# Kernel optimization log

Measured on AMD Instinct MI355X. Metric: run time of the kernel, lower is better.

The kernel has to match this reference:

```python
import jax, jax.numpy as jnp
import numpy as np

B, S, D = 32, 512, 768
V = 8192          # codebook size
K = 8             # mixing samples per position
DP_NOISE_SCALE = 0.1


def setup_inputs() -> dict:
    key = jax.random.key(0)
    k1, k2, k3, k4 = jax.random.split(key, 4)
    base_embeddings = jax.random.normal(k1, (B, S, D), dtype=jnp.float32)
    codebook = jax.random.normal(k2, (V, D), dtype=jnp.float32)
    # stands in for the torch Laplace(0, dp_noise_scale) sample; unit-scale laplace here,
    # scaled by DP_NOISE_SCALE inside reference
    noise = jax.random.laplace(k3, (B, S, D), dtype=jnp.float32)
    # stands in for np.random.randint(batch_size) drawn per (b, s, k)
    rand_idx = jax.random.randint(k4, (B, S, K), 0, B, dtype=jnp.int32)
    return {"base_embeddings": base_embeddings, "codebook": codebook,
            "noise": noise, "rand_idx": rand_idx}


def reference(base_embeddings, codebook, noise, rand_idx):
    # --- VQ quantize: nearest codebook entry per token -----------------
    cb_sq = jnp.sum(codebook * codebook, axis=-1)              # [V]
    dots = jnp.einsum('bsd,vd->bsv', base_embeddings, codebook)  # [B,S,V]
    idx = jnp.argmin(cb_sq[None, None, :] - 2.0 * dots, axis=-1)  # [B,S] int

    # --- random cross-batch mixing of codebook vectors -----------------
    # mixed[b,s] = mean_j codebook[ idx[rand_idx[b,s,j], s] ]
    s_ar = jnp.arange(S)[None, :, None]                         # [1,S,1]
    gathered_idx = idx[rand_idx, s_ar]                          # [B,S,K]
    mixed = jnp.mean(codebook[gathered_idx], axis=2)            # [B,S,D]

    # --- DP laplace noise ----------------------------------------------
    mixed = mixed + DP_NOISE_SCALE * noise
    return mixed
```

## Files before the change

### kernel.cpp

```cpp
#include <hip/hip_runtime.h>
#include <hip/hip_bf16.h>
#include <cstdint>

#define BB 32
#define SS 512
#define DD 768
#define VV 8192
#define KK 8
#define TT (BB * SS)
#define NOISE_SCALE 0.1f

#define BM 128
#define BN 128
#define BK 32
#define NS 8
#define NTL ((VV / NS) / BN)
#define NKC (DD / BK)
#define DELTA 0.25f

using short8  = __attribute__((ext_vector_type(8))) short;
using ushort8 = __attribute__((ext_vector_type(8))) unsigned short;
using f32x4   = __attribute__((ext_vector_type(4))) float;

__global__ void cbsq_kernel(const float* __restrict__ cb, float* __restrict__ cbsq) {
    int row  = blockIdx.x * 4 + (threadIdx.x >> 6);
    int lane = threadIdx.x & 63;
    const float4* p = reinterpret_cast<const float4*>(cb + (size_t)row * DD);
    float s = 0.f;
#pragma unroll
    for (int w = 0; w < 3; ++w) {
        float4 v = p[lane + 64 * w];
        s += v.x * v.x + v.y * v.y + v.z * v.z + v.w * v.w;
    }
#pragma unroll
    for (int off = 32; off; off >>= 1) s += __shfl_xor(s, off, 64);
    if (lane == 0) cbsq[row] = s;
}

__device__ __forceinline__ void top2_ins(float s, int n, float& s1, int& i1,
                                         float& s2, int& i2) {
    if (s < s1 || (s == s1 && n < i1)) { s2 = s1; i2 = i1; s1 = s; i1 = n; }
    else if (s < s2 || (s == s2 && n < i2)) { s2 = s; i2 = n; }
}

__device__ __forceinline__ void bfsplit(float v, unsigned short& h, unsigned short& l) {
    uint u = __float_as_uint(v);
    h = (unsigned short)(u >> 16);
    float r = v - __uint_as_float(u & 0xffff0000u);
    l = (unsigned short)(__float_as_uint(r) >> 16);
}

__device__ __forceinline__ int swz(int row, int slot) {
    return slot ^ ((row ^ (row >> 2)) & 3);
}

__global__ __launch_bounds__(256) void conv_kernel(
    const float* __restrict__ src, unsigned short* __restrict__ hi,
    unsigned short* __restrict__ lo) {
    int i = blockIdx.x * 256 + threadIdx.x;
    float4 v = reinterpret_cast<const float4*>(src)[i];
    ushort4 h, l;
    bfsplit(v.x, h.x, l.x); bfsplit(v.y, h.y, l.y);
    bfsplit(v.z, h.z, l.z); bfsplit(v.w, h.w, l.w);
    reinterpret_cast<ushort4*>(hi)[i] = h;
    reinterpret_cast<ushort4*>(lo)[i] = l;
}

template <bool PRECONV>
__global__ __launch_bounds__(256, 2) void argmin_mfma(
    const float* __restrict__ X,
    const float* __restrict__ CB,
    const unsigned short* __restrict__ Xh, const unsigned short* __restrict__ Xl,
    const unsigned short* __restrict__ CBh, const unsigned short* __restrict__ CBl,
    const float* __restrict__ cbsq,
    float4* __restrict__ part)
{
    __shared__ unsigned short Ah[BM * BK], Al[BM * BK], Bh[BM * BK], Bl[BM * BK];

    const int tid  = threadIdx.x;
    const int lane = tid & 63;
    const int wid  = tid >> 6;
    const int wm = wid >> 1, wn = wid & 1;
    const int l15 = lane & 15, lg = lane >> 4;
    const int mtile = blockIdx.x >> 3;
    const int ns    = blockIdx.x & 7;
    const int m0 = mtile * BM;

    float s1[16], s2[16]; int i1[16], i2[16];
#pragma unroll
    for (int j = 0; j < 16; ++j) {
        s1[j] = INFINITY; s2[j] = INFINITY; i1[j] = 0x7fffffff; i2[j] = 0x7fffffff;
    }

    for (int nt = 0; nt < NTL; ++nt) {
        const int n1 = ns * (VV / NS) + nt * BN;

        f32x4 acc[4][4];
#pragma unroll
        for (int mt = 0; mt < 4; ++mt)
#pragma unroll
            for (int nf = 0; nf < 4; ++nf) acc[mt][nf] = (f32x4){0.f, 0.f, 0.f, 0.f};

        for (int kc = 0; kc < NKC; ++kc) {
            if constexpr (PRECONV) {
                const unsigned short* Agh = Xh  + (size_t)m0 * DD + kc * BK;
                const unsigned short* Agl = Xl  + (size_t)m0 * DD + kc * BK;
                const unsigned short* Bgh = CBh + (size_t)n1 * DD + kc * BK;
                const unsigned short* Bgl = CBl + (size_t)n1 * DD + kc * BK;
#pragma unroll
                for (int i = 0; i < 2; ++i) {
                    int e = tid + 256 * i;
                    int row = e >> 2, q = e & 3;
                    int so = row * BK + (swz(row, q) << 3);
                    size_t go = (size_t)row * DD + q * 8;
                    *reinterpret_cast<ushort8*>(&Ah[so]) = *reinterpret_cast<const ushort8*>(Agh + go);
                    *reinterpret_cast<ushort8*>(&Al[so]) = *reinterpret_cast<const ushort8*>(Agl + go);
                    *reinterpret_cast<ushort8*>(&Bh[so]) = *reinterpret_cast<const ushort8*>(Bgh + go);
                    *reinterpret_cast<ushort8*>(&Bl[so]) = *reinterpret_cast<const ushort8*>(Bgl + go);
                }
            } else {
                const float* Ag = X  + (size_t)m0 * DD + kc * BK;
                const float* Bg = CB + (size_t)n1 * DD + kc * BK;
#pragma unroll
                for (int i = 0; i < 4; ++i) {
                    int e = tid + 256 * i;
                    int row = e >> 3, kq = (e & 7) << 2;
                    int so = row * BK + (swz(row, kq >> 3) << 3) + (kq & 7);
                    float4 va = *reinterpret_cast<const float4*>(Ag + (size_t)row * DD + kq);
                    ushort4 ha, la;
                    bfsplit(va.x, ha.x, la.x); bfsplit(va.y, ha.y, la.y);
                    bfsplit(va.z, ha.z, la.z); bfsplit(va.w, ha.w, la.w);
                    *reinterpret_cast<ushort4*>(&Ah[so]) = ha;
                    *reinterpret_cast<ushort4*>(&Al[so]) = la;
                    float4 vb = *reinterpret_cast<const float4*>(Bg + (size_t)row * DD + kq);
                    ushort4 hb, lb;
                    bfsplit(vb.x, hb.x, lb.x); bfsplit(vb.y, hb.y, lb.y);
                    bfsplit(vb.z, hb.z, lb.z); bfsplit(vb.w, hb.w, lb.w);
                    *reinterpret_cast<ushort4*>(&Bh[so]) = hb;
                    *reinterpret_cast<ushort4*>(&Bl[so]) = lb;
                }
            }
            __syncthreads();

            short8 ah[4], al[4];
#pragma unroll
            for (int mt = 0; mt < 4; ++mt) {
                int row = wm * 64 + mt * 16 + l15;
                int fo  = row * BK + (swz(row, lg) << 3);
                ah[mt] = *reinterpret_cast<const short8*>(&Ah[fo]);
                al[mt] = *reinterpret_cast<const short8*>(&Al[fo]);
            }
#pragma unroll
            for (int nf = 0; nf < 4; ++nf) {
                int row = wn * 64 + nf * 16 + l15;
                int fo  = row * BK + (swz(row, lg) << 3);
                short8 bh = *reinterpret_cast<const short8*>(&Bh[fo]);
                short8 bl = *reinterpret_cast<const short8*>(&Bl[fo]);
#pragma unroll
                for (int mt = 0; mt < 4; ++mt) {
                    acc[mt][nf] = __builtin_amdgcn_mfma_f32_16x16x32_bf16(ah[mt], bh, acc[mt][nf], 0, 0, 0);
                    acc[mt][nf] = __builtin_amdgcn_mfma_f32_16x16x32_bf16(ah[mt], bl, acc[mt][nf], 0, 0, 0);
                    acc[mt][nf] = __builtin_amdgcn_mfma_f32_16x16x32_bf16(al[mt], bh, acc[mt][nf], 0, 0, 0);
                }
            }
            __syncthreads();
        }

        float cq[4]; int nn[4];
#pragma unroll
        for (int nf = 0; nf < 4; ++nf) {
            nn[nf] = n1 + wn * 64 + nf * 16 + l15;
            cq[nf] = cbsq[nn[nf]];
        }
#pragma unroll
        for (int mt = 0; mt < 4; ++mt)
#pragma unroll
            for (int r = 0; r < 4; ++r) {
                const int j = mt * 4 + r;
#pragma unroll
                for (int nf = 0; nf < 4; ++nf) {
                    float s = fmaf(-2.f, acc[mt][nf][r], cq[nf]);
                    top2_ins(s, nn[nf], s1[j], i1[j], s2[j], i2[j]);
                }
            }
    }

#pragma unroll
    for (int st = 1; st < 16; st <<= 1) {
#pragma unroll
        for (int j = 0; j < 16; ++j) {
            float os1 = __shfl_xor(s1[j], st, 64); int oi1 = __shfl_xor(i1[j], st, 64);
            float os2 = __shfl_xor(s2[j], st, 64); int oi2 = __shfl_xor(i2[j], st, 64);
            top2_ins(os1, oi1, s1[j], i1[j], s2[j], i2[j]);
            top2_ins(os2, oi2, s1[j], i1[j], s2[j], i2[j]);
        }
    }
    if (l15 == 0) {
#pragma unroll
        for (int j = 0; j < 16; ++j) {
            int mt = j >> 2, r = j & 3;
            int token = m0 + wm * 64 + mt * 16 + lg * 4 + r;
            part[(size_t)(ns * 2 + wn) * TT + token] =
                make_float4(s1[j], s2[j], __int_as_float(i1[j]), __int_as_float(i2[j]));
        }
    }
}

__global__ __launch_bounds__(256) void rescue_kernel(
    const float* __restrict__ X, const float* __restrict__ CB,
    const float* __restrict__ cbsq, const float4* __restrict__ part,
    int* __restrict__ idx)
{
    int wv = threadIdx.x >> 6, lane = threadIdx.x & 63;
    int t = blockIdx.x * 4 + wv;

    float s1 = INFINITY, s2 = INFINITY; int j1 = 0x7fffffff, j2 = 0x7fffffff;
    if (lane < 16) {
        float4 p = part[(size_t)lane * TT + t];
        s1 = p.x; s2 = p.y; j1 = __float_as_int(p.z); j2 = __float_as_int(p.w);
    }
#pragma unroll
    for (int st = 1; st < 16; st <<= 1) {
        float os1 = __shfl_xor(s1, st, 64); int oi1 = __shfl_xor(j1, st, 64);
        float os2 = __shfl_xor(s2, st, 64); int oi2 = __shfl_xor(j2, st, 64);
        top2_ins(os1, oi1, s1, j1, s2, j2);
        top2_ins(os2, oi2, s1, j1, s2, j2);
    }
    s1 = __shfl(s1, 0, 64); s2 = __shfl(s2, 0, 64);
    j1 = __shfl(j1, 0, 64); j2 = __shfl(j2, 0, 64);

    int res;
    if (s2 - s1 > DELTA) {
        res = j1;
    } else {
        const float* x  = X  + (size_t)t * DD;
        const float* c1 = CB + (size_t)j1 * DD;
        const float* c2 = CB + (size_t)j2 * DD;
        float p1 = 0.f, p2 = 0.f;
#pragma unroll
        for (int q = 0; q < 12; ++q) {
            int d = lane + 64 * q;
            p1 = fmaf(x[d], c1[d], p1);
            p2 = fmaf(x[d], c2[d], p2);
        }
#pragma unroll
        for (int off = 32; off; off >>= 1) {
            p1 += __shfl_xor(p1, off, 64);
            p2 += __shfl_xor(p2, off, 64);
        }
        float e1 = fmaf(-2.f, p1, cbsq[j1]);
        float e2 = fmaf(-2.f, p2, cbsq[j2]);
        res = (e1 < e2 || (e1 == e2 && j1 < j2)) ? j1 : j2;
    }
    if (lane == 0) idx[t] = res;
}

__global__ __launch_bounds__(256) void mix_kernel(
    const float* __restrict__ CB,
    const float* __restrict__ noise,
    const int*   __restrict__ ridx,
    const int*   __restrict__ idx,
    float* __restrict__ out)
{
    int wave = threadIdx.x >> 6;
    int lane = threadIdx.x & 63;
    int t = blockIdx.x * 4 + wave;
    int s = t & (SS - 1);

    const int* r = ridx + (size_t)t * KK;
    const float4* nz = reinterpret_cast<const float4*>(noise + (size_t)t * DD);
    float4* o = reinterpret_cast<float4*>(out + (size_t)t * DD);

    const float4* rows[KK];
#pragma unroll
    for (int j = 0; j < KK; ++j) {
        int g = idx[r[j] * SS + s];
        rows[j] = reinterpret_cast<const float4*>(CB + (size_t)g * DD);
    }

#pragma unroll
    for (int w = 0; w < 3; ++w) {
        int p = lane + 64 * w;
        float4 a = {0.f, 0.f, 0.f, 0.f};
#pragma unroll
        for (int j = 0; j < KK; ++j) {
            float4 c = rows[j][p];
            a.x += c.x; a.y += c.y; a.z += c.z; a.w += c.w;
        }
        float4 nv = nz[p];
        float4 res;
        res.x = a.x * 0.125f + NOISE_SCALE * nv.x;
        res.y = a.y * 0.125f + NOISE_SCALE * nv.y;
        res.z = a.z * 0.125f + NOISE_SCALE * nv.z;
        res.w = a.w * 0.125f + NOISE_SCALE * nv.w;
        o[p] = res;
    }
}

extern "C" void kernel_launch(void* const* d_in, const int* in_sizes, int n_in,
                              void* d_out, int out_size, void* d_ws, size_t ws_size,
                              hipStream_t stream) {
    const float* base  = (const float*)d_in[0];
    const float* cb    = (const float*)d_in[1];
    const float* noise = (const float*)d_in[2];
    const int*   ridx  = (const int*)d_in[3];
    float* out = (float*)d_out;

    char* w = (char*)d_ws;
    float*  cbsq = (float*)w;                 w += (size_t)VV * 4;
    float4* part = (float4*)w;                w += (size_t)2 * NS * TT * 16;
    int*    idx  = (int*)w;                   w += (size_t)TT * 4;
    unsigned short* Xh  = (unsigned short*)w; w += (size_t)TT * DD * 2;
    unsigned short* Xl  = (unsigned short*)w; w += (size_t)TT * DD * 2;
    unsigned short* CBh = (unsigned short*)w; w += (size_t)VV * DD * 2;
    unsigned short* CBl = (unsigned short*)w; w += (size_t)VV * DD * 2;
    const size_t need = (size_t)(w - (char*)d_ws);

    cbsq_kernel<<<VV / 4, 256, 0, stream>>>(cb, cbsq);

    if (ws_size >= need) {
        conv_kernel<<<(TT * DD / 4) / 256, 256, 0, stream>>>(base, Xh, Xl);
        conv_kernel<<<(VV * DD / 4) / 256, 256, 0, stream>>>(cb, CBh, CBl);
        argmin_mfma<true><<<(TT / BM) * NS, 256, 0, stream>>>(
            base, cb, Xh, Xl, CBh, CBl, cbsq, part);
    } else {
        argmin_mfma<false><<<(TT / BM) * NS, 256, 0, stream>>>(
            base, cb, nullptr, nullptr, nullptr, nullptr, cbsq, part);
    }

    rescue_kernel<<<TT / 4, 256, 0, stream>>>(base, cb, cbsq, part, idx);
    mix_kernel<<<TT / 4, 256, 0, stream>>>(cb, noise, ridx, idx, out);
}
```

Before: 1.658 ms.

## Pre-tile operands and double-buffer LDS with async global_load_lds in argmin GEMM

The conversion kernels now write bf16 hi/lo planes in a pre-swizzled, tile-contiguous layout, so the GEMM can copy whole tiles straight into LDS with global_load_lds. The argmin kernel flattens the nt/kc loops into one stream of steps and double-buffers LDS, prefetching the next tile while MFMAs run on the current one, with one barrier per step. This removes the register round trip for staging and hides load latency. The cost is twice the LDS per block, and the launch_bounds occupancy hint of 2 blocks per CU is dropped.

```diff
diff --git a/kernel.cpp b/kernel.cpp
--- a/kernel.cpp
+++ b/kernel.cpp
@@ -16,11 +16,18 @@
 #define NS 8
 #define NTL ((VV / NS) / BN)
 #define NKC (DD / BK)
+#define NSTEP (NTL * NKC)
+#define PLANE_USH 4096
+#define TILE_USH 8192
 #define DELTA 0.25f
 
 using short8  = __attribute__((ext_vector_type(8))) short;
 using ushort8 = __attribute__((ext_vector_type(8))) unsigned short;
 using f32x4   = __attribute__((ext_vector_type(4))) float;
+
+#define GLOAD_LDS16(l, g) __builtin_amdgcn_global_load_lds(                    \
+    (__attribute__((address_space(1))) void*)(g),                              \
+    (__attribute__((address_space(3))) void*)(l), 16, 0, 0)
 
 __global__ void cbsq_kernel(const float* __restrict__ cb, float* __restrict__ cbsq) {
     int row  = blockIdx.x * 4 + (threadIdx.x >> 6);
@@ -54,28 +61,35 @@
     return slot ^ ((row ^ (row >> 2)) & 3);
 }
 
-__global__ __launch_bounds__(256) void conv_kernel(
-    const float* __restrict__ src, unsigned short* __restrict__ hi,
-    unsigned short* __restrict__ lo) {
-    int i = blockIdx.x * 256 + threadIdx.x;
-    float4 v = reinterpret_cast<const float4*>(src)[i];
-    ushort4 h, l;
-    bfsplit(v.x, h.x, l.x); bfsplit(v.y, h.y, l.y);
-    bfsplit(v.z, h.z, l.z); bfsplit(v.w, h.w, l.w);
-    reinterpret_cast<ushort4*>(hi)[i] = h;
-    reinterpret_cast<ushort4*>(lo)[i] = l;
-}
-
-template <bool PRECONV>
-__global__ __launch_bounds__(256, 2) void argmin_mfma(
-    const float* __restrict__ X,
-    const float* __restrict__ CB,
-    const unsigned short* __restrict__ Xh, const unsigned short* __restrict__ Xl,
-    const unsigned short* __restrict__ CBh, const unsigned short* __restrict__ CBl,
+__global__ __launch_bounds__(256) void conv_tiled(const float* __restrict__ src,
+                                                  unsigned short* __restrict__ dst) {
+    int e = blockIdx.x * 256 + threadIdx.x;
+    int tile = e >> 9, inner = e & 511;
+    int row = inner >> 2, slot = inner & 3;
+    int rt = tile / NKC, kc = tile - rt * NKC;
+    const float* sp = src + (size_t)(rt * BM + row) * DD + kc * BK + slot * 8;
+    float4 v0 = *reinterpret_cast<const float4*>(sp);
+    float4 v1 = *reinterpret_cast<const float4*>(sp + 4);
+    float vv[8] = {v0.x, v0.y, v0.z, v0.w, v1.x, v1.y, v1.z, v1.w};
+    ushort8 h, l;
+#pragma unroll
+    for (int i = 0; i < 8; ++i) {
+        unsigned short hh, ll;
+        bfsplit(vv[i], hh, ll);
+        h[i] = hh; l[i] = ll;
+    }
+    size_t base = (size_t)tile * TILE_USH + row * BK + swz(row, slot) * 8;
+    *reinterpret_cast<ushort8*>(dst + base) = h;
+    *reinterpret_cast<ushort8*>(dst + base + PLANE_USH) = l;
+}
+
+__global__ __launch_bounds__(256) void argmin_async(
+    const unsigned short* __restrict__ Axt,
+    const unsigned short* __restrict__ Bxt,
     const float* __restrict__ cbsq,
     float4* __restrict__ part)
 {
-    __shared__ unsigned short Ah[BM * BK], Al[BM * BK], Bh[BM * BK], Bl[BM * BK];
+    __shared__ unsigned short lds[2][4][PLANE_USH];
 
     const int tid  = threadIdx.x;
     const int lane = tid & 63;
@@ -92,56 +106,149 @@
         s1[j] = INFINITY; s2[j] = INFINITY; i1[j] = 0x7fffffff; i2[j] = 0x7fffffff;
     }
 
+    f32x4 acc[4][4];
+#pragma unroll
+    for (int mt = 0; mt < 4; ++mt)
+#pragma unroll
+        for (int nf = 0; nf < 4; ++nf) acc[mt][nf] = (f32x4){0.f, 0.f, 0.f, 0.f};
+
+    auto stage = [&](int b, int snt, int skc) {
+        const unsigned short* src = (wid < 2)
+            ? Axt + (size_t)(mtile * NKC + skc) * TILE_USH
+            : Bxt + (size_t)((ns * NTL + snt) * NKC + skc) * TILE_USH;
+        src += (wid & 1) * PLANE_USH + lane * 8;
+        unsigned short* dst = &lds[b][wid][0];
+#pragma unroll
+        for (int c = 0; c < 8; ++c)
+            GLOAD_LDS16(dst + c * 512, src + c * 512);
+    };
+
+    stage(0, 0, 0);
+    __syncthreads();
+
+    int cur = 0, nt = 0, kc = 0;
+    for (int s = 0; s < NSTEP; ++s) {
+        int nnt = nt, nkc = kc + 1;
+        if (nkc == NKC) { nkc = 0; ++nnt; }
+        if (s + 1 < NSTEP) stage(cur ^ 1, nnt, nkc);
+
+        const unsigned short (&L)[4][PLANE_USH] = lds[cur];
+        short8 ah[4], al[4];
+#pragma unroll
+        for (int mt = 0; mt < 4; ++mt) {
+            int row = wm * 64 + mt * 16 + l15;
+            int fo  = row * BK + swz(row, lg) * 8;
+            ah[mt] = *reinterpret_cast<const short8*>(&L[0][fo]);
+            al[mt] = *reinterpret_cast<const short8*>(&L[1][fo]);
+        }
+#pragma unroll
+        for (int nf = 0; nf < 4; ++nf) {
+            int row = wn * 64 + nf * 16 + l15;
+            int fo  = row * BK + swz(row, lg) * 8;
+            short8 bh = *reinterpret_cast<const short8*>(&L[2][fo]);
+            short8 bl = *reinterpret_cast<const short8*>(&L[3][fo]);
+#pragma unroll
+            for (int mt = 0; mt < 4; ++mt) {
+                acc[mt][nf] = __builtin_amdgcn_mfma_f32_16x16x32_bf16(ah[mt], bh, acc[mt][nf], 0, 0, 0);
+                acc[mt][nf] = __builtin_amdgcn_mfma_f32_16x16x32_bf16(ah[mt], bl, acc[mt][nf], 0, 0, 0);
+                acc[mt][nf] = __builtin_amdgcn_mfma_f32_16x16x32_bf16(al[mt], bh, acc[mt][nf], 0, 0, 0);
+            }
+        }
+
+        if (kc == NKC - 1) {
+            int n1 = ns * (VV / NS) + nt * BN;
+            float cq[4]; int nn[4];
+#pragma unroll
+            for (int nf = 0; nf < 4; ++nf) {
+                nn[nf] = n1 + wn * 64 + nf * 16 + l15;
+                cq[nf] = cbsq[nn[nf]];
+            }
+#pragma unroll
+            for (int mt = 0; mt < 4; ++mt)
+#pragma unroll
+                for (int r = 0; r < 4; ++r) {
+                    const int j = mt * 4 + r;
+#pragma unroll
+                    for (int nf = 0; nf < 4; ++nf) {
+                        float sc = fmaf(-2.f, acc[mt][nf][r], cq[nf]);
+                        top2_ins(sc, nn[nf], s1[j], i1[j], s2[j], i2[j]);
+                    }
+                }
+#pragma unroll
+            for (int mt = 0; mt < 4; ++mt)
+#pragma unroll
+                for (int nf = 0; nf < 4; ++nf) acc[mt][nf] = (f32x4){0.f, 0.f, 0.f, 0.f};
+        }
+        __syncthreads();
+        cur ^= 1; nt = nnt; kc = nkc;
+    }
+
+#pragma unroll
+    for (int st = 1; st < 16; st <<= 1) {
+#pragma unroll
+        for (int j = 0; j < 16; ++j) {
+            float os1 = __shfl_xor(s1[j], st, 64); int oi1 = __shfl_xor(i1[j], st, 64);
+            float os2 = __shfl_xor(s2[j], st, 64); int oi2 = __shfl_xor(i2[j], st, 64);
+            top2_ins(os1, oi1, s1[j], i1[j], s2[j], i2[j]);
+            top2_ins(os2, oi2, s1[j], i1[j], s2[j], i2[j]);
+        }
+    }
+    if (l15 == 0) {
+#pragma unroll
+        for (int j = 0; j < 16; ++j) {
+            int mt = j >> 2, r = j & 3;
+            int token = m0 + wm * 64 + mt * 16 + lg * 4 + r;
+            part[(size_t)(ns * 2 + wn) * TT + token] =
+                make_float4(s1[j], s2[j], __int_as_float(i1[j]), __int_as_float(i2[j]));
+        }
+    }
+}
+
+__global__ __launch_bounds__(256) void argmin_fb(
+    const float* __restrict__ X, const float* __restrict__ CB,
+    const float* __restrict__ cbsq, float4* __restrict__ part)
+{
+    __shared__ unsigned short Ah[BM * BK], Al[BM * BK], Bh[BM * BK], Bl[BM * BK];
+    const int tid = threadIdx.x, lane = tid & 63, wid = tid >> 6;
+    const int wm = wid >> 1, wn = wid & 1;
+    const int l15 = lane & 15, lg = lane >> 4;
+    const int mtile = blockIdx.x >> 3, ns = blockIdx.x & 7;
+    const int m0 = mtile * BM;
+
+    float s1[16], s2[16]; int i1[16], i2[16];
+#pragma unroll
+    for (int j = 0; j < 16; ++j) {
+        s1[j] = INFINITY; s2[j] = INFINITY; i1[j] = 0x7fffffff; i2[j] = 0x7fffffff;
+    }
     for (int nt = 0; nt < NTL; ++nt) {
         const int n1 = ns * (VV / NS) + nt * BN;
-
         f32x4 acc[4][4];
 #pragma unroll
         for (int mt = 0; mt < 4; ++mt)
 #pragma unroll
             for (int nf = 0; nf < 4; ++nf) acc[mt][nf] = (f32x4){0.f, 0.f, 0.f, 0.f};
-
         for (int kc = 0; kc < NKC; ++kc) {
-            if constexpr (PRECONV) {
-                const unsigned short* Agh = Xh  + (size_t)m0 * DD + kc * BK;
-                const unsigned short* Agl = Xl  + (size_t)m0 * DD + kc * BK;
-                const unsigned short* Bgh = CBh + (size_t)n1 * DD + kc * BK;
-                const unsigned short* Bgl = CBl + (size_t)n1 * DD + kc * BK;
-#pragma unroll
-                for (int i = 0; i < 2; ++i) {
-                    int e = tid + 256 * i;
-                    int row = e >> 2, q = e & 3;
-                    int so = row * BK + (swz(row, q) << 3);
-                    size_t go = (size_t)row * DD + q * 8;
-                    *reinterpret_cast<ushort8*>(&Ah[so]) = *reinterpret_cast<const ushort8*>(Agh + go);
-                    *reinterpret_cast<ushort8*>(&Al[so]) = *reinterpret_cast<const ushort8*>(Agl + go);
-                    *reinterpret_cast<ushort8*>(&Bh[so]) = *reinterpret_cast<const ushort8*>(Bgh + go);
-                    *reinterpret_cast<ushort8*>(&Bl[so]) = *reinterpret_cast<const ushort8*>(Bgl + go);
-                }
-            } else {
-                const float* Ag = X  + (size_t)m0 * DD + kc * BK;
-                const float* Bg = CB + (size_t)n1 * DD + kc * BK;
-#pragma unroll
-                for (int i = 0; i < 4; ++i) {
-                    int e = tid + 256 * i;
-                    int row = e >> 3, kq = (e & 7) << 2;
-                    int so = row * BK + (swz(row, kq >> 3) << 3) + (kq & 7);
-                    float4 va = *reinterpret_cast<const float4*>(Ag + (size_t)row * DD + kq);
-                    ushort4 ha, la;
-                    bfsplit(va.x, ha.x, la.x); bfsplit(va.y, ha.y, la.y);
-                    bfsplit(va.z, ha.z, la.z); bfsplit(va.w, ha.w, la.w);
-                    *reinterpret_cast<ushort4*>(&Ah[so]) = ha;
-                    *reinterpret_cast<ushort4*>(&Al[so]) = la;
-                    float4 vb = *reinterpret_cast<const float4*>(Bg + (size_t)row * DD + kq);
-                    ushort4 hb, lb;
-                    bfsplit(vb.x, hb.x, lb.x); bfsplit(vb.y, hb.y, lb.y);
-                    bfsplit(vb.z, hb.z, lb.z); bfsplit(vb.w, hb.w, lb.w);
-                    *reinterpret_cast<ushort4*>(&Bh[so]) = hb;
-                    *reinterpret_cast<ushort4*>(&Bl[so]) = lb;
-                }
+            const float* Ag = X  + (size_t)m0 * DD + kc * BK;
+            const float* Bg = CB + (size_t)n1 * DD + kc * BK;
+#pragma unroll
+            for (int i = 0; i < 4; ++i) {
+                int e = tid + 256 * i;
+                int row = e >> 3, kq = (e & 7) << 2;
+                int so = row * BK + (swz(row, kq >> 3) << 3) + (kq & 7);
+                float4 va = *reinterpret_cast<const float4*>(Ag + (size_t)row * DD + kq);
+                ushort4 ha, la;
+                bfsplit(va.x, ha.x, la.x); bfsplit(va.y, ha.y, la.y);
+                bfsplit(va.z, ha.z, la.z); bfsplit(va.w, ha.w, la.w);
+                *reinterpret_cast<ushort4*>(&Ah[so]) = ha;
+                *reinterpret_cast<ushort4*>(&Al[so]) = la;
+                float4 vb = *reinterpret_cast<const float4*>(Bg + (size_t)row * DD + kq);
+                ushort4 hb, lb;
+                bfsplit(vb.x, hb.x, lb.x); bfsplit(vb.y, hb.y, lb.y);
+                bfsplit(vb.z, hb.z, lb.z); bfsplit(vb.w, hb.w, lb.w);
+                *reinterpret_cast<ushort4*>(&Bh[so]) = hb;
+                *reinterpret_cast<ushort4*>(&Bl[so]) = lb;
             }
             __syncthreads();
-
             short8 ah[4], al[4];
 #pragma unroll
             for (int mt = 0; mt < 4; ++mt) {
@@ -165,7 +272,6 @@
             }
             __syncthreads();
         }
-
         float cq[4]; int nn[4];
 #pragma unroll
         for (int nf = 0; nf < 4; ++nf) {
@@ -179,12 +285,11 @@
                 const int j = mt * 4 + r;
 #pragma unroll
                 for (int nf = 0; nf < 4; ++nf) {
-                    float s = fmaf(-2.f, acc[mt][nf][r], cq[nf]);
-                    top2_ins(s, nn[nf], s1[j], i1[j], s2[j], i2[j]);
+                    float sc = fmaf(-2.f, acc[mt][nf][r], cq[nf]);
+                    top2_ins(sc, nn[nf], s1[j], i1[j], s2[j], i2[j]);
                 }
             }
     }
-
 #pragma unroll
     for (int st = 1; st < 16; st <<= 1) {
 #pragma unroll
@@ -310,22 +415,18 @@
     float*  cbsq = (float*)w;                 w += (size_t)VV * 4;
     float4* part = (float4*)w;                w += (size_t)2 * NS * TT * 16;
     int*    idx  = (int*)w;                   w += (size_t)TT * 4;
-    unsigned short* Xh  = (unsigned short*)w; w += (size_t)TT * DD * 2;
-    unsigned short* Xl  = (unsigned short*)w; w += (size_t)TT * DD * 2;
-    unsigned short* CBh = (unsigned short*)w; w += (size_t)VV * DD * 2;
-    unsigned short* CBl = (unsigned short*)w; w += (size_t)VV * DD * 2;
+    unsigned short* Axt = (unsigned short*)w; w += (size_t)128 * NKC * TILE_USH * 2;
+    unsigned short* Bxt = (unsigned short*)w; w += (size_t)64  * NKC * TILE_USH * 2;
     const size_t need = (size_t)(w - (char*)d_ws);
 
     cbsq_kernel<<<VV / 4, 256, 0, stream>>>(cb, cbsq);
 
     if (ws_size >= need) {
-        conv_kernel<<<(TT * DD / 4) / 256, 256, 0, stream>>>(base, Xh, Xl);
-        conv_kernel<<<(VV * DD / 4) / 256, 256, 0, stream>>>(cb, CBh, CBl);
-        argmin_mfma<true><<<(TT / BM) * NS, 256, 0, stream>>>(
-            base, cb, Xh, Xl, CBh, CBl, cbsq, part);
+        conv_tiled<<<(128 * NKC * 512) / 256, 256, 0, stream>>>(base, Axt);
+        conv_tiled<<<(64  * NKC * 512) / 256, 256, 0, stream>>>(cb, Bxt);
+        argmin_async<<<(TT / BM) * NS, 256, 0, stream>>>(Axt, Bxt, cbsq, part);
     } else {
-        argmin_mfma<false><<<(TT / BM) * NS, 256, 0, stream>>>(
-            base, cb, nullptr, nullptr, nullptr, nullptr, cbsq, part);
+        argmin_fb<<<(TT / BM) * NS, 256, 0, stream>>>(base, cb, cbsq, part);
     }
 
     rescue_kernel<<<TT / 4, 256, 0, stream>>>(base, cb, cbsq, part, idx);
```

New measurement: 1.587 ms. -4.2%, faster.
